# Performance work log

Measured on AMD Instinct MI355X. Metric: run time of the kernel, lower is better.

## Reference

```python
import jax, jax.numpy as jnp
import numpy as np

M, K, N, GROUP = 32, 8192, 28672, 128


def setup_inputs() -> dict:
    key = jax.random.key(0)
    k1, k2, k3, k4 = jax.random.split(key, 4)
    x = jax.random.normal(k1, (M, K), dtype=jnp.float16)
    # int32 words, each packing 8 consecutive int4 values along K
    qweight = jax.random.randint(k2, (K // 8, N), 0, 2147483647, dtype=jnp.int32)
    scales = (jax.random.uniform(k3, (K // GROUP, N), dtype=jnp.float32) * 0.01 + 0.001).astype(jnp.float16)
    bias = (jax.random.normal(k4, (N,), dtype=jnp.float32) * 0.02).astype(jnp.float16)
    return {"x": x, "qweight": qweight, "scales": scales, "bias": bias}


def reference(x, qweight, scales, bias):
    # Unpack 8 int4 nibbles per int32 word along K: (K//8, N) -> (K, N)
    K8, n = qweight.shape
    shifts = (jnp.arange(8, dtype=jnp.int32) * 4)[None, :, None]
    wq = ((qweight[:, None, :] >> shifts) & 15).reshape(K8 * 8, n)  # [K, N] in [0,15]
    # Dequant: zero-point fixed at 8 (pack() asserts zeros==8), per-group scales
    w = wq.astype(jnp.float16) - jnp.float16(8.0)
    g, gs = scales.shape[0], (K8 * 8) // scales.shape[0]
    w = (w.reshape(g, gs, n) * scales[:, None, :]).reshape(K8 * 8, n)  # [K, N] fp16
    return jnp.dot(x, w) + bias  # [M, N]
```

## Files before the change

### kernel.cpp

```cpp
#include <hip/hip_runtime.h>
#include <stdint.h>

#define K_DIM 8192
#define N_DIM 28672

typedef _Float16 half8 __attribute__((ext_vector_type(8)));
typedef _Float16 half2t __attribute__((ext_vector_type(2)));
typedef float f32x16 __attribute__((ext_vector_type(16)));

__global__ __launch_bounds__(256) void prep_x(const float* __restrict__ x,
                                              _Float16* __restrict__ xp) {
  int idx = blockIdx.x * 256 + threadIdx.x;
  int m  = idx & 31;
  int k8 = idx >> 5;
  const float* p = x + (size_t)m * K_DIM + (size_t)k8 * 8;
  float4 xa = *(const float4*)p;
  float4 xb = *(const float4*)(p + 4);
  half2t p0 = __builtin_bit_cast(half2t, __builtin_amdgcn_cvt_pkrtz(xa.x, xb.x));
  half2t p1 = __builtin_bit_cast(half2t, __builtin_amdgcn_cvt_pkrtz(xa.y, xb.y));
  half2t p2 = __builtin_bit_cast(half2t, __builtin_amdgcn_cvt_pkrtz(xa.z, xb.z));
  half2t p3 = __builtin_bit_cast(half2t, __builtin_amdgcn_cvt_pkrtz(xa.w, xb.w));
  half8 o;
  o[0] = p0[0]; o[1] = p0[1]; o[2] = p1[0]; o[3] = p1[1];
  o[4] = p2[0]; o[5] = p2[1]; o[6] = p3[0]; o[7] = p3[1];
  *(half8*)(xp + ((size_t)k8 * 32 + m) * 8) = o;
}

static __device__ __forceinline__ half8 dqs(uint32_t w, half2t sh) {
  const uint32_t M4 = 0x000F000Fu, E = 0x64006400u;
  half2t off; off[0] = (_Float16)(-1032.0f); off[1] = (_Float16)(-1032.0f);
  half2t v0 = (__builtin_bit_cast(half2t, ( w        & M4) | E) + off) * sh;
  half2t v1 = (__builtin_bit_cast(half2t, ((w >> 4)  & M4) | E) + off) * sh;
  half2t v2 = (__builtin_bit_cast(half2t, ((w >> 8)  & M4) | E) + off) * sh;
  half2t v3 = (__builtin_bit_cast(half2t, ((w >> 12) & M4) | E) + off) * sh;
  half8 r;
  r[0] = v0[0]; r[1] = v0[1]; r[2] = v1[0]; r[3] = v1[1];
  r[4] = v2[0]; r[5] = v2[1]; r[6] = v3[0]; r[7] = v3[1];
  return r;
}

static __device__ __forceinline__ void group_step(
    bool prefetch, const _Float16*& ap, const float*& sp, const uint32_t*& qpre,
    uint32_t (&wcur)[8], uint32_t (&wnext)[8], f32x16& acc) {
  half8 af[8];
#pragma unroll
  for (int i = 0; i < 8; i++)
    af[i] = *(const half8*)(ap + (size_t)(2 * i) * 256);
  float s = sp[0];
  half2t sh = __builtin_bit_cast(half2t, __builtin_amdgcn_cvt_pkrtz(s, s));
  if (prefetch) {
#pragma unroll
    for (int i = 0; i < 8; i++) wnext[i] = qpre[(size_t)(2 * i) * N_DIM];
    qpre += (size_t)16 * N_DIM;
  }
#pragma unroll
  for (int i = 0; i < 8; i++)
    acc = __builtin_amdgcn_mfma_f32_32x32x16_f16(af[i], dqs(wcur[i], sh), acc, 0, 0, 0);
  ap += (size_t)16 * 256;
  sp += N_DIM;
}

__global__ __launch_bounds__(512, 6) void qgemm(
    const uint32_t* __restrict__ q, const float* __restrict__ scales,
    const float* __restrict__ bias, const _Float16* __restrict__ xp,
    float* __restrict__ out) {
  __shared__ float red[8][32][32];
  const int tid  = threadIdx.x;
  const int wave = tid >> 6;
  const int lane = tid & 63;
  const int h    = lane >> 5;
  const int nl   = lane & 31;
  const int col0 = blockIdx.x << 5;

  const int wr0 = wave << 7;

  const uint32_t* qcur = q + (size_t)(wr0 + h) * N_DIM + col0 + nl;
  const _Float16* ap   = xp + ((size_t)(wr0 + h) * 32 + nl) * 8;
  const float*    sp   = scales + (size_t)(wave << 3) * N_DIM + col0 + nl;

  f32x16 acc;
#pragma unroll
  for (int j = 0; j < 16; j++) acc[j] = 0.0f;

  uint32_t wA[8], wB[8];
#pragma unroll
  for (int i = 0; i < 8; i++) wA[i] = qcur[(size_t)(2 * i) * N_DIM];
  const uint32_t* qpre = qcur + (size_t)16 * N_DIM;

  for (int gg = 0; gg < 4; ++gg) {
    group_step(true,    ap, sp, qpre, wA, wB, acc);
    group_step(gg < 3,  ap, sp, qpre, wB, wA, acc);
  }

#pragma unroll
  for (int j = 0; j < 16; j++) {
    int row = (j & 3) + ((j >> 2) << 3) + (h << 2);
    red[wave][row][nl] = acc[j];
  }
  __syncthreads();

  const int col = tid & 31;
  const int r0  = tid >> 5;
#pragma unroll
  for (int i = 0; i < 2; i++) {
    int row = r0 + (i << 4);
    float v = 0.0f;
#pragma unroll
    for (int w = 0; w < 8; w++) v += red[w][row][col];
    v += bias[col0 + col];
    out[(size_t)row * N_DIM + col0 + col] = v;
  }
}

extern "C" void kernel_launch(void* const* d_in, const int* in_sizes, int n_in,
                              void* d_out, int out_size, void* d_ws, size_t ws_size,
                              hipStream_t stream) {
  const float*    xf      = (const float*)d_in[0];
  const uint32_t* qweight = (const uint32_t*)d_in[1];
  const float*    scales  = (const float*)d_in[2];
  const float*    bias    = (const float*)d_in[3];
  float*          out     = (float*)d_out;
  _Float16*       xp      = (_Float16*)d_ws;

  prep_x<<<dim3(128), dim3(256), 0, stream>>>(xf, xp);
  qgemm<<<dim3(N_DIM / 32), dim3(512), 0, stream>>>(qweight, scales, bias, xp, out);
}
```

Measured before the change: 212.9 us.

## Split-K across blocks with LDS triple-buffered async loads and atomic reduction

Replaces the intra-block 8-wave split-K reduction through LDS with a split-K across 8 blocks, each covering 128 columns with 4 waves. The x and packed weight tiles are staged into LDS with global_load_lds in a 3-deep ring, using manual vmcnt waits and barriers. Partial sums are combined with float atomics into an output that a new kernel zeros first. This aims to hide global latency and widen weight loads, at the cost of an extra launch, atomic traffic and non-deterministic summation order.

```diff
diff --git a/kernel.cpp b/kernel.cpp
--- a/kernel.cpp
+++ b/kernel.cpp
@@ -26,6 +26,10 @@
   *(half8*)(xp + ((size_t)k8 * 32 + m) * 8) = o;
 }
 
+__global__ __launch_bounds__(256) void zero_out(float4* __restrict__ out) {
+  out[(size_t)blockIdx.x * 256 + threadIdx.x] = float4{0.f, 0.f, 0.f, 0.f};
+}
+
 static __device__ __forceinline__ half8 dqs(uint32_t w, half2t sh) {
   const uint32_t M4 = 0x000F000Fu, E = 0x64006400u;
   half2t off; off[0] = (_Float16)(-1032.0f); off[1] = (_Float16)(-1032.0f);
@@ -39,76 +43,86 @@
   return r;
 }
 
-static __device__ __forceinline__ void group_step(
-    bool prefetch, const _Float16*& ap, const float*& sp, const uint32_t*& qpre,
-    uint32_t (&wcur)[8], uint32_t (&wnext)[8], f32x16& acc) {
-  half8 af[8];
-#pragma unroll
-  for (int i = 0; i < 8; i++)
-    af[i] = *(const half8*)(ap + (size_t)(2 * i) * 256);
-  float s = sp[0];
-  half2t sh = __builtin_bit_cast(half2t, __builtin_amdgcn_cvt_pkrtz(s, s));
-  if (prefetch) {
-#pragma unroll
-    for (int i = 0; i < 8; i++) wnext[i] = qpre[(size_t)(2 * i) * N_DIM];
-    qpre += (size_t)16 * N_DIM;
-  }
-#pragma unroll
-  for (int i = 0; i < 8; i++)
-    acc = __builtin_amdgcn_mfma_f32_32x32x16_f16(af[i], dqs(wcur[i], sh), acc, 0, 0, 0);
-  ap += (size_t)16 * 256;
-  sp += N_DIM;
+static __device__ __forceinline__ void gl_lds16(const void* g, void* l) {
+  __builtin_amdgcn_global_load_lds(
+      (const __attribute__((address_space(1))) uint32_t*)g,
+      (__attribute__((address_space(3))) uint32_t*)l, 16, 0, 0);
 }
 
-__global__ __launch_bounds__(512, 6) void qgemm(
+static __device__ __forceinline__ void waitcnt_vm(int n) {
+  switch (n) {
+    case 0: __builtin_amdgcn_s_waitcnt(0x0F70); break;
+    case 4: __builtin_amdgcn_s_waitcnt(0x0F74); break;
+    default: __builtin_amdgcn_s_waitcnt(0x0F78); break;
+  }
+}
+
+__global__ __launch_bounds__(256, 4) void qgemm(
     const uint32_t* __restrict__ q, const float* __restrict__ scales,
     const float* __restrict__ bias, const _Float16* __restrict__ xp,
     float* __restrict__ out) {
-  __shared__ float red[8][32][32];
+  __shared__ __attribute__((aligned(16))) char smem[3 * 16384];
   const int tid  = threadIdx.x;
-  const int wave = tid >> 6;
+  const int w    = tid >> 6;
   const int lane = tid & 63;
   const int h    = lane >> 5;
   const int nl   = lane & 31;
-  const int col0 = blockIdx.x << 5;
+  const int bid  = blockIdx.x;
+  const int kblk = bid & 7;
+  const int col0 = (bid >> 3) << 7;
+  const int wr0  = kblk << 7;
+  const int colw = col0 + (w << 5);
 
-  const int wr0 = wave << 7;
+  half2t sh[8];
+#pragma unroll
+  for (int g = 0; g < 8; g++) {
+    float s = scales[(size_t)(kblk * 8 + g) * N_DIM + colw + nl];
+    sh[g] = __builtin_bit_cast(half2t, __builtin_amdgcn_cvt_pkrtz(s, s));
+  }
 
-  const uint32_t* qcur = q + (size_t)(wr0 + h) * N_DIM + col0 + nl;
-  const _Float16* ap   = xp + ((size_t)(wr0 + h) * 32 + nl) * 8;
-  const float*    sp   = scales + (size_t)(wave << 3) * N_DIM + col0 + nl;
+  const char* xb = (const char*)xp;
+  auto stage = [&](int g) {
+    char* A = smem + (g % 3) * 16384;
+    char* Q = A + 8192;
+    size_t ga = (size_t)(wr0 + 16 * g) * 512 + (size_t)w * 2048 + (size_t)lane * 16;
+#pragma unroll
+    for (int j = 0; j < 2; j++)
+      gl_lds16(xb + ga + j * 1024, A + w * 2048 + j * 1024);
+#pragma unroll
+    for (int j = 0; j < 2; j++) {
+      int row = wr0 + 16 * g + 4 * w + 2 * j + h;
+      gl_lds16(q + (size_t)row * N_DIM + col0 + nl * 4, Q + (4 * w + 2 * j) * 512);
+    }
+  };
 
   f32x16 acc;
 #pragma unroll
   for (int j = 0; j < 16; j++) acc[j] = 0.0f;
 
-  uint32_t wA[8], wB[8];
+  stage(0); stage(1); stage(2);
+
 #pragma unroll
-  for (int i = 0; i < 8; i++) wA[i] = qcur[(size_t)(2 * i) * N_DIM];
-  const uint32_t* qpre = qcur + (size_t)16 * N_DIM;
-
-  for (int gg = 0; gg < 4; ++gg) {
-    group_step(true,    ap, sp, qpre, wA, wB, acc);
-    group_step(gg < 3,  ap, sp, qpre, wB, wA, acc);
+  for (int g = 0; g < 8; g++) {
+    waitcnt_vm(g <= 5 ? 8 : (g == 6 ? 4 : 0));
+    __builtin_amdgcn_s_barrier();
+    const char* A = smem + (g % 3) * 16384;
+    const char* Q = A + 8192;
+    half2t s = sh[g];
+#pragma unroll
+    for (int i = 0; i < 8; i++) {
+      half8 af = *(const half8*)(A + (size_t)((2 * i + h) * 32 + nl) * 16);
+      uint32_t wq = *(const uint32_t*)(Q + (2 * i + h) * 512 + (w * 32 + nl) * 4);
+      acc = __builtin_amdgcn_mfma_f32_32x32x16_f16(af, dqs(wq, s), acc, 0, 0, 0);
+    }
+    __builtin_amdgcn_s_barrier();
+    if (g + 3 < 8) stage(g + 3);
   }
 
+  float bs = (kblk == 0) ? bias[colw + nl] : 0.0f;
 #pragma unroll
   for (int j = 0; j < 16; j++) {
     int row = (j & 3) + ((j >> 2) << 3) + (h << 2);
-    red[wave][row][nl] = acc[j];
-  }
-  __syncthreads();
-
-  const int col = tid & 31;
-  const int r0  = tid >> 5;
-#pragma unroll
-  for (int i = 0; i < 2; i++) {
-    int row = r0 + (i << 4);
-    float v = 0.0f;
-#pragma unroll
-    for (int w = 0; w < 8; w++) v += red[w][row][col];
-    v += bias[col0 + col];
-    out[(size_t)row * N_DIM + col0 + col] = v;
+    unsafeAtomicAdd(&out[(size_t)row * N_DIM + colw + nl], acc[j] + bs);
   }
 }
 
@@ -122,6 +136,7 @@
   float*          out     = (float*)d_out;
   _Float16*       xp      = (_Float16*)d_ws;
 
+  zero_out<<<dim3(896), dim3(256), 0, stream>>>((float4*)out);
   prep_x<<<dim3(128), dim3(256), 0, stream>>>(xf, xp);
-  qgemm<<<dim3(N_DIM / 32), dim3(512), 0, stream>>>(qweight, scales, bias, xp, out);
+  qgemm<<<dim3((N_DIM / 128) * 8), dim3(256), 0, stream>>>(qweight, scales, bias, xp, out);
 }
```

After: 189.5 us. -11.0%, faster.

## Split K across blocks with atomic accumulation and LDS-staged activations

Applied to the files above, without the earlier changes.

Replaces the per-block in-block K reduction with a split-K grid of 7168 small blocks, each covering 256 K rows for 128 columns, and combines their partial sums through float atomics into an output pre-filled with bias by a new init kernel. Activations are staged into shared memory with direct global-to-LDS loads, and each wave loads all 16 weight words up front instead of double-buffering. The aim is more parallelism and latency hiding for the memory-bound weight stream. The cost is 32-way atomic contention on every output element, an extra kernel launch, and nondeterministic summation order.

```diff
diff --git a/kernel.cpp b/kernel.cpp
--- a/kernel.cpp
+++ b/kernel.cpp
@@ -26,6 +26,13 @@
   *(half8*)(xp + ((size_t)k8 * 32 + m) * 8) = o;
 }
 
+__global__ __launch_bounds__(256) void init_out(const float* __restrict__ bias,
+                                                float* __restrict__ out) {
+  int idx = blockIdx.x * 256 + threadIdx.x;
+  int n = idx % N_DIM;
+  out[idx] = bias[n];
+}
+
 static __device__ __forceinline__ half8 dqs(uint32_t w, half2t sh) {
   const uint32_t M4 = 0x000F000Fu, E = 0x64006400u;
   half2t off; off[0] = (_Float16)(-1032.0f); off[1] = (_Float16)(-1032.0f);
@@ -39,76 +46,62 @@
   return r;
 }
 
-static __device__ __forceinline__ void group_step(
-    bool prefetch, const _Float16*& ap, const float*& sp, const uint32_t*& qpre,
-    uint32_t (&wcur)[8], uint32_t (&wnext)[8], f32x16& acc) {
-  half8 af[8];
-#pragma unroll
-  for (int i = 0; i < 8; i++)
-    af[i] = *(const half8*)(ap + (size_t)(2 * i) * 256);
-  float s = sp[0];
-  half2t sh = __builtin_bit_cast(half2t, __builtin_amdgcn_cvt_pkrtz(s, s));
-  if (prefetch) {
-#pragma unroll
-    for (int i = 0; i < 8; i++) wnext[i] = qpre[(size_t)(2 * i) * N_DIM];
-    qpre += (size_t)16 * N_DIM;
-  }
-#pragma unroll
-  for (int i = 0; i < 8; i++)
-    acc = __builtin_amdgcn_mfma_f32_32x32x16_f16(af[i], dqs(wcur[i], sh), acc, 0, 0, 0);
-  ap += (size_t)16 * 256;
-  sp += N_DIM;
+static __device__ __forceinline__ void gl_lds16(const void* g, void* l) {
+  __builtin_amdgcn_global_load_lds(
+      (const __attribute__((address_space(1))) uint32_t*)g,
+      (__attribute__((address_space(3))) uint32_t*)l, 16, 0, 0);
 }
 
-__global__ __launch_bounds__(512, 6) void qgemm(
+__global__ __launch_bounds__(256, 8) void qgemm(
     const uint32_t* __restrict__ q, const float* __restrict__ scales,
-    const float* __restrict__ bias, const _Float16* __restrict__ xp,
-    float* __restrict__ out) {
-  __shared__ float red[8][32][32];
+    const _Float16* __restrict__ xp, float* __restrict__ out) {
+  __shared__ __attribute__((aligned(16))) char Abuf[16384];
   const int tid  = threadIdx.x;
-  const int wave = tid >> 6;
+  const int w    = tid >> 6;
   const int lane = tid & 63;
   const int h    = lane >> 5;
   const int nl   = lane & 31;
-  const int col0 = blockIdx.x << 5;
+  const int bid  = blockIdx.x;
+  const int ks   = bid & 31;
+  const int col0 = (bid >> 5) << 7;
+  const int colw = col0 + (w << 5);
+  const int kr0  = ks << 5;
 
-  const int wr0 = wave << 7;
+  float s0f = scales[(size_t)(ks * 2)     * N_DIM + colw + nl];
+  float s1f = scales[(size_t)(ks * 2 + 1) * N_DIM + colw + nl];
 
-  const uint32_t* qcur = q + (size_t)(wr0 + h) * N_DIM + col0 + nl;
-  const _Float16* ap   = xp + ((size_t)(wr0 + h) * 32 + nl) * 8;
-  const float*    sp   = scales + (size_t)(wave << 3) * N_DIM + col0 + nl;
+  {
+    const char* src = (const char*)xp + (size_t)kr0 * 512 + w * 4096 + (size_t)lane * 16;
+    char* dst = Abuf + w * 4096;
+#pragma unroll
+    for (int j = 0; j < 4; j++) gl_lds16(src + j * 1024, dst + j * 1024);
+  }
+
+  uint32_t wq[16];
+  const uint32_t* qp = q + (size_t)(kr0 + h) * N_DIM + colw + nl;
+#pragma unroll
+  for (int i = 0; i < 16; i++) wq[i] = qp[(size_t)(2 * i) * N_DIM];
+
+  __syncthreads();
+
+  half2t sh0 = __builtin_bit_cast(half2t, __builtin_amdgcn_cvt_pkrtz(s0f, s0f));
+  half2t sh1 = __builtin_bit_cast(half2t, __builtin_amdgcn_cvt_pkrtz(s1f, s1f));
 
   f32x16 acc;
 #pragma unroll
   for (int j = 0; j < 16; j++) acc[j] = 0.0f;
 
-  uint32_t wA[8], wB[8];
 #pragma unroll
-  for (int i = 0; i < 8; i++) wA[i] = qcur[(size_t)(2 * i) * N_DIM];
-  const uint32_t* qpre = qcur + (size_t)16 * N_DIM;
-
-  for (int gg = 0; gg < 4; ++gg) {
-    group_step(true,    ap, sp, qpre, wA, wB, acc);
-    group_step(gg < 3,  ap, sp, qpre, wB, wA, acc);
+  for (int i = 0; i < 16; i++) {
+    half8 af = *(const half8*)(Abuf + (size_t)(((2 * i + h) * 32) + nl) * 16);
+    acc = __builtin_amdgcn_mfma_f32_32x32x16_f16(af, dqs(wq[i], i < 8 ? sh0 : sh1),
+                                                 acc, 0, 0, 0);
   }
 
 #pragma unroll
   for (int j = 0; j < 16; j++) {
     int row = (j & 3) + ((j >> 2) << 3) + (h << 2);
-    red[wave][row][nl] = acc[j];
-  }
-  __syncthreads();
-
-  const int col = tid & 31;
-  const int r0  = tid >> 5;
-#pragma unroll
-  for (int i = 0; i < 2; i++) {
-    int row = r0 + (i << 4);
-    float v = 0.0f;
-#pragma unroll
-    for (int w = 0; w < 8; w++) v += red[w][row][col];
-    v += bias[col0 + col];
-    out[(size_t)row * N_DIM + col0 + col] = v;
+    unsafeAtomicAdd(&out[(size_t)row * N_DIM + colw + nl], acc[j]);
   }
 }
 
@@ -122,6 +115,7 @@
   float*          out     = (float*)d_out;
   _Float16*       xp      = (_Float16*)d_ws;
 
+  init_out<<<dim3(3584), dim3(256), 0, stream>>>(bias, out);
   prep_x<<<dim3(128), dim3(256), 0, stream>>>(xf, xp);
-  qgemm<<<dim3(N_DIM / 32), dim3(512), 0, stream>>>(qweight, scales, bias, xp, out);
+  qgemm<<<dim3(224 * 32), dim3(256), 0, stream>>>(qweight, scales, xp, out);
 }
```

After: 239.0 us. +12.2%, slower.

## Halve split-K waves per block and deepen weight prefetch to three stages

Applied to the files above, without the earlier changes.

Each block now uses 4 waves instead of 8, with each wave covering 2048 K rows (16 groups) instead of 1024. The loop is fully unrolled with a triple-buffered weight prefetch two groups ahead and double-buffered activation and scale loads one group ahead. This aims to hide more global-memory latency per wave and shrink the shared-memory reduction. In exchange it uses more registers, leaves fewer waves per block, and gives longer serial chains per wave, which may lower memory-level parallelism.

```diff
diff --git a/kernel.cpp b/kernel.cpp
--- a/kernel.cpp
+++ b/kernel.cpp
@@ -39,76 +39,78 @@
   return r;
 }
 
-static __device__ __forceinline__ void group_step(
-    bool prefetch, const _Float16*& ap, const float*& sp, const uint32_t*& qpre,
-    uint32_t (&wcur)[8], uint32_t (&wnext)[8], f32x16& acc) {
-  half8 af[8];
-#pragma unroll
-  for (int i = 0; i < 8; i++)
-    af[i] = *(const half8*)(ap + (size_t)(2 * i) * 256);
-  float s = sp[0];
-  half2t sh = __builtin_bit_cast(half2t, __builtin_amdgcn_cvt_pkrtz(s, s));
-  if (prefetch) {
-#pragma unroll
-    for (int i = 0; i < 8; i++) wnext[i] = qpre[(size_t)(2 * i) * N_DIM];
-    qpre += (size_t)16 * N_DIM;
-  }
-#pragma unroll
-  for (int i = 0; i < 8; i++)
-    acc = __builtin_amdgcn_mfma_f32_32x32x16_f16(af[i], dqs(wcur[i], sh), acc, 0, 0, 0);
-  ap += (size_t)16 * 256;
-  sp += N_DIM;
-}
-
-__global__ __launch_bounds__(512, 6) void qgemm(
+__global__ __launch_bounds__(256, 4) void qgemm(
     const uint32_t* __restrict__ q, const float* __restrict__ scales,
     const float* __restrict__ bias, const _Float16* __restrict__ xp,
     float* __restrict__ out) {
-  __shared__ float red[8][32][32];
+  __shared__ float red[4][32][32];
   const int tid  = threadIdx.x;
-  const int wave = tid >> 6;
+  const int w    = tid >> 6;
   const int lane = tid & 63;
   const int h    = lane >> 5;
   const int nl   = lane & 31;
   const int col0 = blockIdx.x << 5;
+  const int wr0  = w << 8;
 
-  const int wr0 = wave << 7;
+  const uint32_t* qp = q + (size_t)(wr0 + h) * N_DIM + col0 + nl;
+  const half8*    ap = (const half8*)xp + (size_t)(wr0 + h) * 32 + nl;
+  const float*    sp = scales + (size_t)(w << 4) * N_DIM + col0 + nl;
 
-  const uint32_t* qcur = q + (size_t)(wr0 + h) * N_DIM + col0 + nl;
-  const _Float16* ap   = xp + ((size_t)(wr0 + h) * 32 + nl) * 8;
-  const float*    sp   = scales + (size_t)(wave << 3) * N_DIM + col0 + nl;
+  uint32_t qb[3][8];
+  half8    ab[2][8];
+  float    sb[2];
+
+  auto loadQ = [&](int g, uint32_t (&dst)[8]) {
+#pragma unroll
+    for (int i = 0; i < 8; i++)
+      dst[i] = qp[(size_t)(16 * g + 2 * i) * N_DIM];
+  };
+  auto loadA = [&](int g, half8 (&dst)[8]) {
+#pragma unroll
+    for (int i = 0; i < 8; i++)
+      dst[i] = ap[(size_t)(16 * g + 2 * i) * 32];
+  };
 
   f32x16 acc;
 #pragma unroll
   for (int j = 0; j < 16; j++) acc[j] = 0.0f;
 
-  uint32_t wA[8], wB[8];
+  loadQ(0, qb[0]);
+  loadA(0, ab[0]);
+  sb[0] = sp[0];
+  loadQ(1, qb[1]);
+
 #pragma unroll
-  for (int i = 0; i < 8; i++) wA[i] = qcur[(size_t)(2 * i) * N_DIM];
-  const uint32_t* qpre = qcur + (size_t)16 * N_DIM;
-
-  for (int gg = 0; gg < 4; ++gg) {
-    group_step(true,    ap, sp, qpre, wA, wB, acc);
-    group_step(gg < 3,  ap, sp, qpre, wB, wA, acc);
+  for (int g = 0; g < 16; g++) {
+    if (g + 1 < 16) {
+      loadA(g + 1, ab[(g + 1) & 1]);
+      sb[(g + 1) & 1] = sp[(size_t)(g + 1) * N_DIM];
+    }
+    if (g + 2 < 16) loadQ(g + 2, qb[(g + 2) % 3]);
+    float s = sb[g & 1];
+    half2t sh = __builtin_bit_cast(half2t, __builtin_amdgcn_cvt_pkrtz(s, s));
+#pragma unroll
+    for (int i = 0; i < 8; i++)
+      acc = __builtin_amdgcn_mfma_f32_32x32x16_f16(
+          ab[g & 1][i], dqs(qb[g % 3][i], sh), acc, 0, 0, 0);
   }
 
 #pragma unroll
   for (int j = 0; j < 16; j++) {
     int row = (j & 3) + ((j >> 2) << 3) + (h << 2);
-    red[wave][row][nl] = acc[j];
+    red[w][row][nl] = acc[j];
   }
   __syncthreads();
 
   const int col = tid & 31;
   const int r0  = tid >> 5;
+  float bz = bias[col0 + col];
 #pragma unroll
-  for (int i = 0; i < 2; i++) {
-    int row = r0 + (i << 4);
-    float v = 0.0f;
-#pragma unroll
-    for (int w = 0; w < 8; w++) v += red[w][row][col];
-    v += bias[col0 + col];
-    out[(size_t)row * N_DIM + col0 + col] = v;
+  for (int i = 0; i < 4; i++) {
+    int row = r0 + (i << 3);
+    float v = red[0][row][col] + red[1][row][col] +
+              red[2][row][col] + red[3][row][col];
+    out[(size_t)row * N_DIM + col0 + col] = v + bz;
   }
 }
 
@@ -123,5 +125,5 @@
   _Float16*       xp      = (_Float16*)d_ws;
 
   prep_x<<<dim3(128), dim3(256), 0, stream>>>(xf, xp);
-  qgemm<<<dim3(N_DIM / 32), dim3(512), 0, stream>>>(qweight, scales, bias, xp, out);
+  qgemm<<<dim3(N_DIM / 32), dim3(256), 0, stream>>>(qweight, scales, bias, xp, out);
 }
```

After: 209.8 us. Within noise of the previous version (-1.5%).
